# Optimization experiments

Hardware: AMD Instinct MI355X
Metric: run time of the kernel (lower is better)

## Reference

```python
import jax, jax.numpy as jnp
import numpy as np

L = 3          # number of Blocks
D = 1024       # embed_dims
H = 16         # headcount
HD = D // H    # head_size = 64
T = 1024       # context_size
V = 32000      # vocabulary_size
B = 2          # batch
EPS = 1e-5


def layernorm(x, g, b):
    m = jnp.mean(x, axis=-1, keepdims=True)
    v = jnp.var(x, axis=-1, keepdims=True)
    return (x - m) * jax.lax.rsqrt(v + EPS) * g + b


def setup_inputs() -> dict:
    key = jax.random.key(0)
    ks = jax.random.split(key, 16)
    s = 0.02
    return {
        "idx": jax.random.randint(ks[0], (B, T), 0, V, dtype=jnp.int64),
        "tok_emb": jax.random.normal(ks[1], (V, D), jnp.float32) * s,
        "pos_emb": jax.random.normal(ks[2], (T, D), jnp.float32) * s,
        # per-layer stacked attention params (equivalent to per-head Linears concatenated)
        "wq": jax.random.normal(ks[3], (L, H, D, HD), jnp.float32) * s,
        "wk": jax.random.normal(ks[4], (L, H, D, HD), jnp.float32) * s,
        "wv": jax.random.normal(ks[5], (L, H, D, HD), jnp.float32) * s,
        "w_proj": jax.random.normal(ks[6], (L, D, D), jnp.float32) * s,
        "b_proj": jnp.zeros((L, D), jnp.float32),
        "w1": jax.random.normal(ks[7], (L, D, 4 * D), jnp.float32) * s,
        "b1": jnp.zeros((L, 4 * D), jnp.float32),
        "w2": jax.random.normal(ks[8], (L, 4 * D, D), jnp.float32) * s,
        "b2": jnp.zeros((L, D), jnp.float32),
        "ln1_g": jnp.ones((L, D), jnp.float32),
        "ln1_b": jnp.zeros((L, D), jnp.float32),
        "ln2_g": jnp.ones((L, D), jnp.float32),
        "ln2_b": jnp.zeros((L, D), jnp.float32),
        "lnf_g": jnp.ones((D,), jnp.float32),
        "lnf_b": jnp.zeros((D,), jnp.float32),
        "w_lm": jax.random.normal(ks[9], (D, V), jnp.float32) * s,
        "b_lm": jnp.zeros((V,), jnp.float32),
    }


def reference(idx, tok_emb, pos_emb, wq, wk, wv, w_proj, b_proj,
              w1, b1, w2, b2, ln1_g, ln1_b, ln2_g, ln2_b,
              lnf_g, lnf_b, w_lm, b_lm):
    Bc, Tc = idx.shape
    x = tok_emb[idx] + pos_emb[:Tc]                  # [B,T,D]
    causal = jnp.tril(jnp.ones((Tc, Tc), dtype=bool))
    scale = HD ** -0.5
    for l in range(L):
        h = layernorm(x, ln1_g[l], ln1_b[l])
        q = jnp.einsum('btd,hdk->bhtk', h, wq[l])
        k = jnp.einsum('btd,hdk->bhtk', h, wk[l])
        v = jnp.einsum('btd,hdk->bhtk', h, wv[l])
        scores = jnp.einsum('bhtk,bhsk->bhts', q, k) * scale
        scores = jnp.where(causal, scores, -jnp.inf)
        w = jax.nn.softmax(scores, axis=-1)          # dropout = identity (eval)
        attn = jnp.einsum('bhts,bhsk->bhtk', w, v)
        attn = attn.transpose(0, 2, 1, 3).reshape(Bc, Tc, H * HD)
        sa = attn @ w_proj[l] + b_proj[l]
        h2 = layernorm(x, ln2_g[l], ln2_b[l])
        ff = jax.nn.relu(h2 @ w1[l] + b1[l]) @ w2[l] + b2[l]
        # faithful to source: NO residual x; y = sa + ffwd only
        x = sa + ff
    x = layernorm(x, lnf_g, lnf_b)
    logits = x @ w_lm + b_lm                         # [B,T,V]
    return logits
```

## Files before the change

### kernel.cpp

```cpp
#include <hip/hip_runtime.h>

#define D_    1024
#define T_    1024
#define H_    16
#define HD_   64
#define NL    3
#define VOC   32000
#define BAT   2
#define MR    (BAT*T_)

typedef unsigned short u16;
typedef unsigned int   u32;
typedef __bf16 bf16x8 __attribute__((ext_vector_type(8)));
typedef float  f32x4  __attribute__((ext_vector_type(4)));

__device__ __forceinline__ u16 f2b(float f){
  u32 u = __float_as_uint(f);
  u += 0x7fffu + ((u >> 16) & 1u);
  return (u16)(u >> 16);
}
__device__ __forceinline__ float blo(u32 w){ return __uint_as_float(w << 16); }
__device__ __forceinline__ float bhi(u32 w){ return __uint_as_float(w & 0xffff0000u); }
__device__ __forceinline__ u32 pk2(float a, float b){ return (u32)f2b(a) | ((u32)f2b(b) << 16); }

__device__ __forceinline__ void gload16(const u16* g, u16* l){
  __builtin_amdgcn_global_load_lds(
      (const __attribute__((address_space(1))) void*)g,
      (__attribute__((address_space(3))) void*)l, 16, 0, 0);
}

__global__ __launch_bounds__(256) void embed_k(const int* __restrict__ idx,
    const float* __restrict__ tok, const float* __restrict__ pos, float* __restrict__ x){
  int bt = blockIdx.x, tid = threadIdx.x;
  int t = bt & (T_-1);
  int tk = idx[bt];
  float4 a = ((const float4*)(tok + (size_t)tk * D_))[tid];
  float4 p = ((const float4*)(pos + (size_t)t  * D_))[tid];
  a.x += p.x; a.y += p.y; a.z += p.z; a.w += p.w;
  ((float4*)(x + (size_t)bt * D_))[tid] = a;
}

__global__ __launch_bounds__(256) void ln_k(const float* __restrict__ x,
    const float* __restrict__ g, const float* __restrict__ b, u16* __restrict__ out){
  int row = blockIdx.x, tid = threadIdx.x;
  float4 v = ((const float4*)(x + (size_t)row * D_))[tid];
  float s = v.x+v.y+v.z+v.w;
  float q = v.x*v.x+v.y*v.y+v.z*v.z+v.w*v.w;
  #pragma unroll
  for (int off = 32; off >= 1; off >>= 1){
    s += __shfl_xor(s, off);
    q += __shfl_xor(q, off);
  }
  __shared__ float ss[4], sq[4];
  int wave = tid >> 6;
  if ((tid & 63) == 0){ ss[wave] = s; sq[wave] = q; }
  __syncthreads();
  s = ss[0]+ss[1]+ss[2]+ss[3];
  q = sq[0]+sq[1]+sq[2]+sq[3];
  float mean = s * (1.f/D_);
  float var  = q * (1.f/D_) - mean*mean;
  float rs = rsqrtf(var + 1e-5f);
  float4 gg = ((const float4*)g)[tid];
  float4 bb = ((const float4*)b)[tid];
  u32 p0 = pk2((v.x-mean)*rs*gg.x+bb.x, (v.y-mean)*rs*gg.y+bb.y);
  u32 p1 = pk2((v.z-mean)*rs*gg.z+bb.z, (v.w-mean)*rs*gg.w+bb.w);
  ((uint2*)(out + (size_t)row * D_))[tid] = make_uint2(p0, p1);
}

__global__ __launch_bounds__(1024) void repack_t_k(const float* __restrict__ src,
    u16* __restrict__ dst, int K, int N, size_t sstride, size_t dstride){
  __shared__ float tile[32][33];
  int l = blockIdx.z;
  const float* s = src + (size_t)l * sstride;
  u16* d = dst + (size_t)l * dstride;
  int n0 = blockIdx.x << 5, k0 = blockIdx.y << 5;
  int tx = threadIdx.x, ty = threadIdx.y;
  tile[ty][tx] = s[(size_t)(k0 + ty) * N + n0 + tx];
  __syncthreads();
  d[(size_t)(n0 + ty) * K + k0 + tx] = f2b(tile[tx][ty]);
}

__global__ __launch_bounds__(1024) void repack_qkv_k(const float* __restrict__ wq,
    const float* __restrict__ wk, const float* __restrict__ wv, u16* __restrict__ dst){
  __shared__ float tile[32][33];
  int l = blockIdx.z;
  int d0 = blockIdx.x << 5;
  int n0 = blockIdx.y << 5;
  int which = n0 >> 10, within = n0 & 1023;
  int hh = within >> 6, hd0 = within & 63;
  const float* src = (which == 0 ? wq : (which == 1 ? wk : wv))
                     + ((size_t)l * H_ + hh) * (D_ * HD_);
  int tx = threadIdx.x, ty = threadIdx.y;
  tile[ty][tx] = src[(size_t)(d0 + ty) * HD_ + hd0 + tx];
  __syncthreads();
  dst[((size_t)l * 3072 + n0 + ty) * D_ + d0 + tx] = f2b(tile[tx][ty]);
}

__global__ __launch_bounds__(256) void gemm_k(
    const u16* __restrict__ A, const u16* __restrict__ Bt,
    const float* __restrict__ bias, const float* __restrict__ resid,
    float* __restrict__ Cf, u16* __restrict__ Cb,
    int M, int N, int K, int relu)
{
  __shared__ __attribute__((aligned(16))) u16 Als[128*32];
  __shared__ __attribute__((aligned(16))) u16 Bls[128*32];
  int tiles_m = M >> 7, tiles_n = N >> 7;
  int tm, tn;
  {
    const int GN = 8;
    int full = tiles_n / GN;
    int fullsz = full * GN * tiles_m;
    int bid = blockIdx.x;
    if (bid < fullsz){
      int g = bid / (GN * tiles_m);
      int r = bid % (GN * tiles_m);
      tm = r / GN; tn = g * GN + (r % GN);
    } else {
      int r = bid - fullsz;
      int remn = tiles_n - full * GN;
      tm = r / remn; tn = full * GN + (r % remn);
    }
  }
  int m0 = tm << 7, n0 = tn << 7;
  int tid = threadIdx.x, lane = tid & 63, wave = tid >> 6;
  int wm = (wave >> 1) << 6, wn = (wave & 1) << 6;
  f32x4 acc[4][4];
  f32x4 zero = {0.f, 0.f, 0.f, 0.f};
  #pragma unroll
  for (int i = 0; i < 4; i++)
    #pragma unroll
    for (int j = 0; j < 4; j++) acc[i][j] = zero;

  int lrow = lane >> 2, lseg = lane & 3;
  int arow = wave*16 + lrow;
  int ssw  = (arow >> 1) & 3;
  int scol = ((lseg ^ ssw) << 3);
  const u16* Ag0 = A  + (size_t)(m0 + arow) * K + scol;
  const u16* Ag1 = Ag0 + (size_t)64 * K;
  const u16* Bg0 = Bt + (size_t)(n0 + arow) * K + scol;
  const u16* Bg1 = Bg0 + (size_t)64 * K;
  u16* Al0 = Als + wave*512;
  u16* Al1 = Als + 64*32 + wave*512;
  u16* Bl0 = Bls + wave*512;
  u16* Bl1 = Bls + 64*32 + wave*512;

  int fr = lane & 15;
  int fqs = (((lane >> 4) ^ ((fr >> 1) & 3)) << 3);
  for (int k0 = 0; k0 < K; k0 += 32){
    __syncthreads();
    gload16(Ag0 + k0, Al0);
    gload16(Ag1 + k0, Al1);
    gload16(Bg0 + k0, Bl0);
    gload16(Bg1 + k0, Bl1);
    __syncthreads();
    bf16x8 af[4], bfr[4];
    #pragma unroll
    for (int i = 0; i < 4; i++) af[i]  = *(const bf16x8*)(Als + (wm + i*16 + fr)*32 + fqs);
    #pragma unroll
    for (int i = 0; i < 4; i++) bfr[i] = *(const bf16x8*)(Bls + (wn + i*16 + fr)*32 + fqs);
    #pragma unroll
    for (int mi = 0; mi < 4; mi++)
      #pragma unroll
      for (int ni = 0; ni < 4; ni++)
        acc[mi][ni] = __builtin_amdgcn_mfma_f32_16x16x32_bf16(af[mi], bfr[ni], acc[mi][ni], 0, 0, 0);
  }
  int cn = lane & 15, rq = (lane >> 4) << 2;
  #pragma unroll
  for (int mi = 0; mi < 4; mi++){
    #pragma unroll
    for (int ni = 0; ni < 4; ni++){
      int c = n0 + wn + ni*16 + cn;
      float bv = bias ? bias[c] : 0.f;
      #pragma unroll
      for (int r = 0; r < 4; r++){
        int rr = m0 + wm + mi*16 + rq + r;
        float v = acc[mi][ni][r] + bv;
        if (resid) v += resid[(size_t)rr * N + c];
        if (relu)  v = fmaxf(v, 0.f);
        if (Cf) Cf[(size_t)rr * N + c] = v;
        if (Cb) Cb[(size_t)rr * N + c] = f2b(v);
      }
    }
  }
}

__global__ __launch_bounds__(256) void attn_k(const u16* __restrict__ qkv, u16* __restrict__ out){
  __shared__ u16 kls[64][72];
  __shared__ u16 vtls[64][72];
  __shared__ u16 pls[4][16][72];
  int bid = blockIdx.x;
  int qt = bid & 15, bh = bid >> 4;
  int h = bh & (H_-1), b = bh >> 4;
  int q0 = qt << 6;
  int tid = threadIdx.x, lane = tid & 63, wave = tid >> 6;
  int fr = lane & 15, fq = (lane >> 4) << 3;
  int cn = fr, rq = (lane >> 4) << 2;

  const u16* qp = qkv + ((size_t)(b*T_ + q0 + wave*16 + fr) * 3072 + h*64);
  bf16x8 qa0 = *(const bf16x8*)(qp + fq);
  bf16x8 qa1 = *(const bf16x8*)(qp + 32 + fq);

  f32x4 acc[4];
  f32x4 zero = {0.f,0.f,0.f,0.f};
  #pragma unroll
  for (int i = 0; i < 4; i++) acc[i] = zero;
  float mrun[4], lrun[4];
  #pragma unroll
  for (int r = 0; r < 4; r++){ mrun[r] = -1e30f; lrun[r] = 0.f; }

  int ldrow = tid >> 3, ldseg = tid & 7;
  const u16* kbase = qkv + ((size_t)(b*T_ + ldrow) * 3072 + 1024 + h*64 + ldseg*8);
  const size_t rstep = (size_t)32 * 3072;

  for (int ch = 0; ch <= qt; ch++){
    const u16* kp = kbase + (size_t)(ch << 6) * 3072;
    uint4 kv0 = *(const uint4*)kp;
    uint4 kv1 = *(const uint4*)(kp + rstep);
    uint4 vv0 = *(const uint4*)(kp + 1024);
    uint4 vv1 = *(const uint4*)(kp + rstep + 1024);
    __syncthreads();
    *(uint4*)(&kls[ldrow][ldseg*8])      = kv0;
    *(uint4*)(&kls[ldrow + 32][ldseg*8]) = kv1;
    union { uint4 u; u16 s[8]; } vu0, vu1; vu0.u = vv0; vu1.u = vv1;
    #pragma unroll
    for (int j = 0; j < 8; j++){
      vtls[ldseg*8 + j][ldrow]      = vu0.s[j];
      vtls[ldseg*8 + j][ldrow + 32] = vu1.s[j];
    }
    __syncthreads();

    f32x4 sf[4];
    #pragma unroll
    for (int ni = 0; ni < 4; ni++) sf[ni] = zero;
    #pragma unroll
    for (int ni = 0; ni < 4; ni++){
      bf16x8 kb0 = *(const bf16x8*)(&kls[ni*16 + fr][fq]);
      bf16x8 kb1 = *(const bf16x8*)(&kls[ni*16 + fr][32 + fq]);
      sf[ni] = __builtin_amdgcn_mfma_f32_16x16x32_bf16(qa0, kb0, sf[ni], 0, 0, 0);
      sf[ni] = __builtin_amdgcn_mfma_f32_16x16x32_bf16(qa1, kb1, sf[ni], 0, 0, 0);
    }

    int s0 = ch << 6;
    float sv[4][4];
    if (ch == qt){
      #pragma unroll
      for (int ni = 0; ni < 4; ni++)
        #pragma unroll
        for (int r = 0; r < 4; r++){
          int srow = s0 + ni*16 + cn;
          int qrow = q0 + wave*16 + rq + r;
          sv[ni][r] = (srow <= qrow) ? sf[ni][r]*0.125f : -1e30f;
        }
    } else {
      #pragma unroll
      for (int ni = 0; ni < 4; ni++)
        #pragma unroll
        for (int r = 0; r < 4; r++) sv[ni][r] = sf[ni][r]*0.125f;
    }

    #pragma unroll
    for (int r = 0; r < 4; r++){
      float mx = fmaxf(fmaxf(sv[0][r], sv[1][r]), fmaxf(sv[2][r], sv[3][r]));
      #pragma unroll
      for (int off = 8; off >= 1; off >>= 1) mx = fmaxf(mx, __shfl_xor(mx, off));
      float mn = fmaxf(mrun[r], mx);
      float al = __expf(mrun[r] - mn);
      mrun[r] = mn;
      float ps = 0.f;
      #pragma unroll
      for (int ni = 0; ni < 4; ni++){
        float p = __expf(sv[ni][r] - mn);
        sv[ni][r] = p; ps += p;
      }
      #pragma unroll
      for (int off = 8; off >= 1; off >>= 1) ps += __shfl_xor(ps, off);
      lrun[r] = lrun[r]*al + ps;
      #pragma unroll
      for (int ni = 0; ni < 4; ni++) acc[ni][r] *= al;
    }

    #pragma unroll
    for (int ni = 0; ni < 4; ni++)
      #pragma unroll
      for (int r = 0; r < 4; r++)
        pls[wave][rq + r][ni*16 + cn] = f2b(sv[ni][r]);
    __syncthreads();

    #pragma unroll
    for (int kk = 0; kk < 2; kk++){
      bf16x8 pa = *(const bf16x8*)(&pls[wave][fr][kk*32 + fq]);
      #pragma unroll
      for (int di = 0; di < 4; di++){
        bf16x8 vb = *(const bf16x8*)(&vtls[di*16 + fr][kk*32 + fq]);
        acc[di] = __builtin_amdgcn_mfma_f32_16x16x32_bf16(pa, vb, acc[di], 0, 0, 0);
      }
    }
  }

  u16* ob = out + ((size_t)(b*T_ + q0 + wave*16) * D_ + h*64);
  #pragma unroll
  for (int r = 0; r < 4; r++){
    float inv = 1.f / lrun[r];
    #pragma unroll
    for (int di = 0; di < 4; di++)
      ob[(size_t)(rq + r) * D_ + di*16 + cn] = f2b(acc[di][r] * inv);
  }
}

extern "C" void kernel_launch(void* const* d_in, const int* in_sizes, int n_in,
                              void* d_out, int out_size, void* d_ws, size_t ws_size,
                              hipStream_t stream){
  (void)in_sizes; (void)n_in; (void)out_size; (void)ws_size;
  const int*   idx     = (const int*)  d_in[0];
  const float* tok_emb = (const float*)d_in[1];
  const float* pos_emb = (const float*)d_in[2];
  const float* wq      = (const float*)d_in[3];
  const float* wk      = (const float*)d_in[4];
  const float* wv      = (const float*)d_in[5];
  const float* w_proj  = (const float*)d_in[6];
  const float* b_proj  = (const float*)d_in[7];
  const float* w1      = (const float*)d_in[8];
  const float* b1      = (const float*)d_in[9];
  const float* w2      = (const float*)d_in[10];
  const float* b2      = (const float*)d_in[11];
  const float* ln1g    = (const float*)d_in[12];
  const float* ln1b    = (const float*)d_in[13];
  const float* ln2g    = (const float*)d_in[14];
  const float* ln2b    = (const float*)d_in[15];
  const float* lnfg    = (const float*)d_in[16];
  const float* lnfb    = (const float*)d_in[17];
  const float* w_lm    = (const float*)d_in[18];
  const float* b_lm    = (const float*)d_in[19];

  char* ws = (char*)d_ws;
  size_t off = 0;
  auto alloc = [&](size_t bytes)->char*{
    char* p = ws + off; off += (bytes + 255) & ~(size_t)255; return p;
  };
  u16*   qkvT  = (u16*)  alloc((size_t)NL*3072*1024*2);
  u16*   projT = (u16*)  alloc((size_t)NL*1024*1024*2);
  u16*   w1T   = (u16*)  alloc((size_t)NL*4096*1024*2);
  u16*   w2T   = (u16*)  alloc((size_t)NL*1024*4096*2);
  u16*   wlmT  = (u16*)  alloc((size_t)VOC*1024*2);
  float* x     = (float*)alloc((size_t)MR*1024*4);
  u16*   hbuf  = (u16*)  alloc((size_t)MR*1024*2);
  u16*   qkvb  = (u16*)  alloc((size_t)MR*3072*2);
  u16*   attnb = (u16*)  alloc((size_t)MR*1024*2);
  float* sa    = (float*)alloc((size_t)MR*1024*4);
  u16*   ff1   = (u16*)  alloc((size_t)MR*4096*2);

  auto gemm = [&](const u16* A, const u16* Bt, const float* bias, const float* resid,
                  float* Cf, u16* Cb, int M, int N, int K, int relu){
    int blocks = (M >> 7) * (N >> 7);
    gemm_k<<<dim3(blocks), dim3(256), 0, stream>>>(A, Bt, bias, resid, Cf, Cb, M, N, K, relu);
  };

  repack_qkv_k<<<dim3(32,96,3),  dim3(32,32), 0, stream>>>(wq, wk, wv, qkvT);
  repack_t_k  <<<dim3(32,32,3),  dim3(32,32), 0, stream>>>(w_proj, projT, 1024, 1024, (size_t)1048576, (size_t)1048576);
  repack_t_k  <<<dim3(128,32,3), dim3(32,32), 0, stream>>>(w1, w1T, 1024, 4096, (size_t)4194304, (size_t)4194304);
  repack_t_k  <<<dim3(32,128,3), dim3(32,32), 0, stream>>>(w2, w2T, 4096, 1024, (size_t)4194304, (size_t)4194304);
  repack_t_k  <<<dim3(1000,32,1),dim3(32,32), 0, stream>>>(w_lm, wlmT, 1024, VOC, (size_t)0, (size_t)0);

  embed_k<<<dim3(MR), dim3(256), 0, stream>>>(idx, tok_emb, pos_emb, x);

  for (int l = 0; l < NL; l++){
    ln_k<<<dim3(MR), dim3(256), 0, stream>>>(x, ln1g + l*1024, ln1b + l*1024, hbuf);
    gemm(hbuf, qkvT + (size_t)l*3072*1024, nullptr, nullptr, nullptr, qkvb, MR, 3072, 1024, 0);
    attn_k<<<dim3(512), dim3(256), 0, stream>>>(qkvb, attnb);
    gemm(attnb, projT + (size_t)l*1048576, b_proj + l*1024, nullptr, sa, nullptr, MR, 1024, 1024, 0);
    ln_k<<<dim3(MR), dim3(256), 0, stream>>>(x, ln2g + l*1024, ln2b + l*1024, hbuf);
    gemm(hbuf, w1T + (size_t)l*4194304, b1 + l*4096, nullptr, nullptr, ff1, MR, 4096, 1024, 1);
    gemm(ff1, w2T + (size_t)l*4194304, b2 + l*1024, sa, x, nullptr, MR, 1024, 4096, 0);
  }
  ln_k<<<dim3(MR), dim3(256), 0, stream>>>(x, lnfg, lnfb, hbuf);
  gemm(hbuf, wlmT, b_lm, nullptr, (float*)d_out, nullptr, MR, VOC, 1024, 0);
}
```

Baseline: 1.682 ms.

## Double-buffer LDS tiles in bf16 GEMM to overlap loads with MFMA

Splits the GEMM's shared-memory A/B tiles into two buffers and issues the global-to-LDS loads for the next K-slice while MFMAs run on the current one. This removes one barrier per K step and is meant to hide global load latency behind compute. LDS use per block doubles to 32 KB, which may lower occupancy. Correctness depends on gload16's completion semantics across the single barrier, and the loop assumes K is a multiple of 64.

```diff
diff --git a/kernel.cpp b/kernel.cpp
--- a/kernel.cpp
+++ b/kernel.cpp
@@ -102,8 +102,10 @@
     float* __restrict__ Cf, u16* __restrict__ Cb,
     int M, int N, int K, int relu)
 {
-  __shared__ __attribute__((aligned(16))) u16 Als[128*32];
-  __shared__ __attribute__((aligned(16))) u16 Bls[128*32];
+  __shared__ __attribute__((aligned(16))) u16 Als0[128*32];
+  __shared__ __attribute__((aligned(16))) u16 Bls0[128*32];
+  __shared__ __attribute__((aligned(16))) u16 Als1[128*32];
+  __shared__ __attribute__((aligned(16))) u16 Bls1[128*32];
   int tiles_m = M >> 7, tiles_n = N >> 7;
   int tm, tn;
   {
@@ -139,31 +141,44 @@
   const u16* Ag1 = Ag0 + (size_t)64 * K;
   const u16* Bg0 = Bt + (size_t)(n0 + arow) * K + scol;
   const u16* Bg1 = Bg0 + (size_t)64 * K;
-  u16* Al0 = Als + wave*512;
-  u16* Al1 = Als + 64*32 + wave*512;
-  u16* Bl0 = Bls + wave*512;
-  u16* Bl1 = Bls + 64*32 + wave*512;
+  int lofs = wave*512;
 
   int fr = lane & 15;
   int fqs = (((lane >> 4) ^ ((fr >> 1) & 3)) << 3);
-  for (int k0 = 0; k0 < K; k0 += 32){
-    __syncthreads();
-    gload16(Ag0 + k0, Al0);
-    gload16(Ag1 + k0, Al1);
-    gload16(Bg0 + k0, Bl0);
-    gload16(Bg1 + k0, Bl1);
-    __syncthreads();
-    bf16x8 af[4], bfr[4];
-    #pragma unroll
-    for (int i = 0; i < 4; i++) af[i]  = *(const bf16x8*)(Als + (wm + i*16 + fr)*32 + fqs);
-    #pragma unroll
-    for (int i = 0; i < 4; i++) bfr[i] = *(const bf16x8*)(Bls + (wn + i*16 + fr)*32 + fqs);
-    #pragma unroll
-    for (int mi = 0; mi < 4; mi++)
-      #pragma unroll
-      for (int ni = 0; ni < 4; ni++)
-        acc[mi][ni] = __builtin_amdgcn_mfma_f32_16x16x32_bf16(af[mi], bfr[ni], acc[mi][ni], 0, 0, 0);
-  }
+
+  #define STAGE(AL, BL, KO) do { \
+    gload16(Ag0 + (KO), (AL) + lofs); \
+    gload16(Ag1 + (KO), (AL) + 64*32 + lofs); \
+    gload16(Bg0 + (KO), (BL) + lofs); \
+    gload16(Bg1 + (KO), (BL) + 64*32 + lofs); \
+  } while(0)
+
+  #define COMPUTE(AL, BL) do { \
+    bf16x8 af[4], bfr[4]; \
+    _Pragma("unroll") \
+    for (int i = 0; i < 4; i++) af[i]  = *(const bf16x8*)((AL) + (wm + i*16 + fr)*32 + fqs); \
+    _Pragma("unroll") \
+    for (int i = 0; i < 4; i++) bfr[i] = *(const bf16x8*)((BL) + (wn + i*16 + fr)*32 + fqs); \
+    _Pragma("unroll") \
+    for (int mi = 0; mi < 4; mi++) \
+      _Pragma("unroll") \
+      for (int ni = 0; ni < 4; ni++) \
+        acc[mi][ni] = __builtin_amdgcn_mfma_f32_16x16x32_bf16(af[mi], bfr[ni], acc[mi][ni], 0, 0, 0); \
+  } while(0)
+
+  STAGE(Als0, Bls0, 0);
+  __syncthreads();
+  for (int k0 = 0; k0 < K; k0 += 64){
+    STAGE(Als1, Bls1, k0 + 32);
+    COMPUTE(Als0, Bls0);
+    __syncthreads();
+    if (k0 + 64 < K) STAGE(Als0, Bls0, k0 + 64);
+    COMPUTE(Als1, Bls1);
+    __syncthreads();
+  }
+  #undef STAGE
+  #undef COMPUTE
+
   int cn = lane & 15, rq = (lane >> 4) << 2;
   #pragma unroll
   for (int mi = 0; mi < 4; mi++){
```

Result: faster. 1.544 ms (-8.3%).
